# Kernel optimization log

Hardware: AMD Instinct MI355X
Metric: run time of the kernel (lower is better)

Reference implementation:

```python
import jax, jax.numpy as jnp
import numpy as np

M, K, N = 131072, 1024, 512


def setup_inputs() -> dict:
    key = jax.random.key(0)
    k1, k2, k3, k4, k5 = jax.random.split(key, 5)
    scale = 0.02
    return {
        "x": jax.random.normal(k1, (M, K), dtype=jnp.float32),
        "w0": jax.random.uniform(k2, (K,), dtype=jnp.float32, minval=0.9, maxval=1.1),
        "w1": jax.random.normal(k3, (K, N), dtype=jnp.float32) * scale,
        "w2": jax.random.normal(k4, (K, N), dtype=jnp.float32) * scale,
        "w3": jax.random.normal(k5, (N, K), dtype=jnp.float32) * scale,
    }


def reference(x, w0, w1, w2, w3):
    # RMSNorm (no eps, matching the kernel): l = rsqrt(mean(x^2))
    l = jax.lax.rsqrt(jnp.sum(x * x, axis=-1) / K)          # [M]
    x1 = x * l[:, None] * w0[None, :]                        # [M, K]
    x2 = x1 @ w1                                             # gate   [M, N]
    y2 = x1 @ w2                                             # up     [M, N]
    x3 = jax.nn.silu(x2) * y2                                # SiLU-gate [M, N]
    out = x3 @ w3                                            # down   [M, K] (skip_connection=False)
    return out
```

## Files before the change

### kernel.cpp

```cpp
#include <hip/hip_runtime.h>
#include <cstdint>

typedef __attribute__((ext_vector_type(4))) float f32x4;
typedef __attribute__((ext_vector_type(8))) short bf16x8;
typedef __attribute__((ext_vector_type(4))) short bf16x4;

#define DEV static __device__ __forceinline__

DEV unsigned short f2bf(float f) {
    union { float f; unsigned int u; } v; v.f = f;
    unsigned int u = v.u;
    return (unsigned short)((u + 0x7FFFu + ((u >> 16) & 1u)) >> 16);
}

DEV void async_cp16(const void* g, void* l) {
    __builtin_amdgcn_global_load_lds(
        (const __attribute__((address_space(1))) unsigned int*)g,
        (__attribute__((address_space(3))) unsigned int*)l,
        16, 0, 0);
}

#define BAR __builtin_amdgcn_s_barrier();
#define SCB __builtin_amdgcn_sched_barrier(0);
#define LGKM0 asm volatile("s_waitcnt lgkmcnt(0)");
#define P1 __builtin_amdgcn_s_setprio(1);
#define P0 __builtin_amdgcn_s_setprio(0);
#define VM0 asm volatile("s_waitcnt vmcnt(0)" ::: "memory");
#define VM2 asm volatile("s_waitcnt vmcnt(2)" ::: "memory");
#define VM3 asm volatile("s_waitcnt vmcnt(3)" ::: "memory");

DEV void stage_A32(const unsigned short* __restrict__ g, long kofs,
                   unsigned short* l, int tid, int gp) {
#pragma unroll
    for (int i = 0; i < 2; ++i) {
        int c = i * 512 + tid;
        int row = c >> 2;
        int ss = (c & 3) ^ ((row >> 1) & 3);
        async_cp16(g + (long)row * gp + kofs + ss * 8,
                   l + (i * 512 + (tid & 448)) * 8);
    }
}
DEV void stage_B32(const unsigned short* __restrict__ g, long kofs,
                   unsigned short* l, int tid, int gp) {
    int row = tid >> 2;
    int ss = (tid & 3) ^ ((row >> 1) & 3);
    async_cp16(g + (long)row * gp + kofs + ss * 8, l + (tid & 448) * 8);
}

template <int NT>
DEV void gemmB(const unsigned short* __restrict__ gA,
               const unsigned short* __restrict__ gB,
               const int gpa, const int gpb, unsigned short* lds,
               f32x4 (&acc)[4][4], const int tid) {
    const int lane = tid & 63;
    const int wv = tid >> 6;
    const int wr = wv >> 1, wc = wv & 1;
    const int lhi = lane >> 4, llo = lane & 15;
    const int sw = (lhi ^ ((llo >> 1) & 3)) << 3;
    const int aoff = (wr * 64 + llo) * 32 + sw;
    const int boff = (wc * 64 + llo) * 32 + sw;

    unsigned short *pa0 = lds, *pa1 = lds + 8192, *pa2 = lds + 16384;
    unsigned short *pb0 = lds + 24576, *pb1 = lds + 28672;

#define MGJ(J)                                                                \
    _Pragma("unroll") for (int i = 0; i < 4; ++i)                             \
    _Pragma("unroll") for (int jj = 0; jj < 2; ++jj)                          \
        acc[i][(J) + jj] = __builtin_amdgcn_mfma_f32_16x16x32_bf16(           \
            af[i], bf[(J) + jj], acc[i][(J) + jj], 0, 0, 0);

    stage_A32(gA, 0, pa0, tid, gpa);
    stage_B32(gB, 0, pb0, tid, gpb);
    stage_A32(gA, 32, pa1, tid, gpa);
    stage_B32(gB, 32, pb1, tid, gpb);
    VM3
    BAR SCB

    bf16x8 af[4], bf[4];
    for (int t = 0; t < NT; ++t) {
        const bool pf1 = (t + 1 < NT);
        const bool pf2 = (t + 2 < NT);
#pragma unroll
        for (int i = 0; i < 4; ++i) af[i] = *(const bf16x8*)&pa0[aoff + i * 512];
        bf[0] = *(const bf16x8*)&pb0[boff];
        bf[1] = *(const bf16x8*)&pb0[boff + 512];
        if (t >= 1 && pf1) stage_B32(gB, (long)(t + 1) * 32, pb1, tid, gpb);
        BAR LGKM0 SCB
        P1 MGJ(0) P0
        BAR
        bf[2] = *(const bf16x8*)&pb0[boff + 1024];
        bf[3] = *(const bf16x8*)&pb0[boff + 1536];
        if (pf2) stage_A32(gA, (long)(t + 2) * 32, pa2, tid, gpa);
        BAR LGKM0 SCB
        P1 MGJ(2) P0
        if (pf1) { if (pf2) { VM2 } else { VM0 } }
        BAR SCB
        unsigned short* tp = pa0; pa0 = pa1; pa1 = pa2; pa2 = tp;
        tp = pb0; pb0 = pb1; pb1 = tp;
    }
#undef MGJ
}

__global__ void prep_w(const float* __restrict__ w0, const float* __restrict__ w1,
                       const float* __restrict__ w2, const float* __restrict__ w3,
                       unsigned short* __restrict__ w12t, unsigned short* __restrict__ w3t) {
    int t = blockIdx.x * 256 + threadIdx.x;
    if (t < 1048576) {
        int n = t >> 10, k = t & 1023;
        const float* src = (n & 1) ? w2 : w1;
        w12t[t] = f2bf(w0[k] * src[k * 512 + (n >> 1)]);
    } else {
        int idx = t - 1048576;
        int j = idx >> 9, n = idx & 511;
        w3t[idx] = f2bf(w3[n * 1024 + j]);
    }
}

__global__ __launch_bounds__(256)
void prep_x(const float* __restrict__ x, unsigned short* __restrict__ xb) {
    const int wv = threadIdx.x >> 6, lane = threadIdx.x & 63;
    const int stride = gridDim.x * 4;
    for (int row = blockIdx.x * 4 + wv; row < 131072; row += stride) {
        const float* xr = x + (long)row * 1024;
        f32x4 v[4];
        float s = 0.f;
#pragma unroll
        for (int c = 0; c < 4; ++c) {
            v[c] = *(const f32x4*)(xr + c * 256 + lane * 4);
            s += v[c].x * v[c].x + v[c].y * v[c].y + v[c].z * v[c].z + v[c].w * v[c].w;
        }
#pragma unroll
        for (int off = 32; off > 0; off >>= 1) s += __shfl_xor(s, off, 64);
        float l = rsqrtf(s * (1.0f / 1024.0f));
        unsigned short* xo = xb + (long)row * 1024;
#pragma unroll
        for (int c = 0; c < 4; ++c) {
            bf16x4 b;
            b.x = (short)f2bf(v[c].x * l);
            b.y = (short)f2bf(v[c].y * l);
            b.z = (short)f2bf(v[c].z * l);
            b.w = (short)f2bf(v[c].w * l);
            *(bf16x4*)(xo + c * 256 + lane * 4) = b;
        }
    }
}

__global__ __launch_bounds__(512, 4)
void gate_gemm(const unsigned short* __restrict__ xb,
               const unsigned short* __restrict__ w12t,
               unsigned short* __restrict__ x3) {
    __shared__ unsigned short lds[32768];
    const int tid = threadIdx.x;
    const int lane = tid & 63;
    const int wv = tid >> 6;
    const int wr = wv >> 1, wc = wv & 1;
    const int lhi = lane >> 4, llo = lane & 15;

    int bid = blockIdx.x;
    int wgid = (bid & 7) * 512 + (bid >> 3);
    const int mt = wgid >> 3, nt = wgid & 7;

    f32x4 acc[4][4];
#pragma unroll
    for (int i = 0; i < 4; ++i)
#pragma unroll
        for (int j = 0; j < 4; ++j) acc[i][j] = (f32x4){0.f, 0.f, 0.f, 0.f};

    gemmB<32>(xb + (long)mt * 256 * 1024, w12t + (long)nt * 128 * 1024,
              1024, 1024, lds, acc, tid);

#pragma unroll
    for (int i = 0; i < 4; ++i)
#pragma unroll
        for (int rr = 0; rr < 4; ++rr) {
            int R = wr * 64 + i * 16 + lhi * 4 + rr;
#pragma unroll
            for (int j = 0; j < 4; ++j) {
                float v = acc[i][j][rr];
                float p = __shfl_xor(v, 1, 64);
                float g = (lane & 1) ? p : v;
                float u = (lane & 1) ? v : p;
                float s = (g / (1.0f + __expf(-g))) * u;
                if (!(lane & 1))
                    lds[R * 72 + wc * 32 + j * 8 + (llo >> 1)] = f2bf(s);
            }
        }
    __syncthreads();
    unsigned short* xg = x3 + (long)(mt * 256) * 512 + nt * 64;
#pragma unroll
    for (int i = 0; i < 4; ++i) {
        int c = i * 512 + tid;
        int row = c >> 3, ch = c & 7;
        *(bf16x8*)(xg + (long)row * 512 + ch * 8) = *(const bf16x8*)&lds[row * 72 + ch * 8];
    }
}

__global__ __launch_bounds__(512, 4)
void down_gemm(const unsigned short* __restrict__ x3,
               const unsigned short* __restrict__ w3t,
               float* __restrict__ out) {
    __shared__ unsigned short lds[32768];
    const int tid = threadIdx.x;
    const int lane = tid & 63;
    const int wv = tid >> 6;
    const int wr = wv >> 1, wc = wv & 1;
    const int lhi = lane >> 4, llo = lane & 15;

    int bid = blockIdx.x;
    int wgid = (bid & 7) * 512 + (bid >> 3);
    const int mt = wgid >> 3, nt = wgid & 7;

    f32x4 acc[4][4];
#pragma unroll
    for (int i = 0; i < 4; ++i)
#pragma unroll
        for (int j = 0; j < 4; ++j) acc[i][j] = (f32x4){0.f, 0.f, 0.f, 0.f};

    gemmB<16>(x3 + (long)mt * 256 * 512, w3t + (long)nt * 128 * 512,
              512, 512, lds, acc, tid);

    float* op = out + (long)(mt * 256) * 1024 + nt * 128;
#pragma unroll
    for (int i = 0; i < 4; ++i)
#pragma unroll
        for (int rr = 0; rr < 4; ++rr) {
            int R = wr * 64 + i * 16 + lhi * 4 + rr;
#pragma unroll
            for (int j = 0; j < 4; ++j)
                op[(long)R * 1024 + wc * 64 + j * 16 + llo] = acc[i][j][rr];
        }
}

extern "C" void kernel_launch(void* const* d_in, const int* in_sizes, int n_in,
                              void* d_out, int out_size, void* d_ws, size_t ws_size,
                              hipStream_t stream) {
    const float* x  = (const float*)d_in[0];
    const float* w0 = (const float*)d_in[1];
    const float* w1 = (const float*)d_in[2];
    const float* w2 = (const float*)d_in[3];
    const float* w3 = (const float*)d_in[4];
    float* out = (float*)d_out;

    unsigned short* w12t = (unsigned short*)d_ws;
    unsigned short* w3t  = w12t + 1024 * 1024;
    unsigned short* x3   = w3t + 1024 * 512;
    unsigned short* xb   = x3 + (size_t)131072 * 512;

    prep_w<<<dim3(6144), dim3(256), 0, stream>>>(w0, w1, w2, w3, w12t, w3t);
    prep_x<<<dim3(2048), dim3(256), 0, stream>>>(x, xb);
    gate_gemm<<<dim3(4096), dim3(512), 0, stream>>>(xb, w12t, x3);
    down_gemm<<<dim3(4096), dim3(512), 0, stream>>>(x3, w3t, out);
}
```

Before: 697.8 us.

## Shrink GEMM workgroup tiles to 128x128 with 4 waves and fewer barriers

Both GEMM kernels now use 256-thread workgroups computing 128x128 output tiles instead of 512 threads over 256x128, doubling the grid and roughly halving LDS per block. A and B staging share one loader, and the per-iteration barrier count drops from four to two by moving the vmcnt wait ahead of the second barrier. The aim is higher occupancy and less synchronisation overhead. The cost is lower data reuse per tile, so more global/L2 traffic for the weight operand, and an added __syncthreads before the epilogue reuses LDS.

```diff
diff --git a/kernel.cpp b/kernel.cpp
--- a/kernel.cpp
+++ b/kernel.cpp
@@ -27,28 +27,22 @@
 #define P0 __builtin_amdgcn_s_setprio(0);
 #define VM0 asm volatile("s_waitcnt vmcnt(0)" ::: "memory");
 #define VM2 asm volatile("s_waitcnt vmcnt(2)" ::: "memory");
-#define VM3 asm volatile("s_waitcnt vmcnt(3)" ::: "memory");
-
-DEV void stage_A32(const unsigned short* __restrict__ g, long kofs,
+#define VM4 asm volatile("s_waitcnt vmcnt(4)" ::: "memory");
+
+DEV void stage_T32(const unsigned short* __restrict__ g, long kofs,
                    unsigned short* l, int tid, int gp) {
 #pragma unroll
     for (int i = 0; i < 2; ++i) {
-        int c = i * 512 + tid;
+        int c = i * 256 + tid;
         int row = c >> 2;
         int ss = (c & 3) ^ ((row >> 1) & 3);
         async_cp16(g + (long)row * gp + kofs + ss * 8,
-                   l + (i * 512 + (tid & 448)) * 8);
-    }
-}
-DEV void stage_B32(const unsigned short* __restrict__ g, long kofs,
-                   unsigned short* l, int tid, int gp) {
-    int row = tid >> 2;
-    int ss = (tid & 3) ^ ((row >> 1) & 3);
-    async_cp16(g + (long)row * gp + kofs + ss * 8, l + (tid & 448) * 8);
+                   l + (i * 256 + (tid & 192)) * 8);
+    }
 }
 
 template <int NT>
-DEV void gemmB(const unsigned short* __restrict__ gA,
+DEV void gemmC(const unsigned short* __restrict__ gA,
                const unsigned short* __restrict__ gB,
                const int gpa, const int gpb, unsigned short* lds,
                f32x4 (&acc)[4][4], const int tid) {
@@ -60,8 +54,8 @@
     const int aoff = (wr * 64 + llo) * 32 + sw;
     const int boff = (wc * 64 + llo) * 32 + sw;
 
-    unsigned short *pa0 = lds, *pa1 = lds + 8192, *pa2 = lds + 16384;
-    unsigned short *pb0 = lds + 24576, *pb1 = lds + 28672;
+    unsigned short *pa0 = lds, *pa1 = lds + 4096, *pa2 = lds + 8192;
+    unsigned short *pb0 = lds + 12288, *pb1 = lds + 16384;
 
 #define MGJ(J)                                                                \
     _Pragma("unroll") for (int i = 0; i < 4; ++i)                             \
@@ -69,11 +63,11 @@
         acc[i][(J) + jj] = __builtin_amdgcn_mfma_f32_16x16x32_bf16(           \
             af[i], bf[(J) + jj], acc[i][(J) + jj], 0, 0, 0);
 
-    stage_A32(gA, 0, pa0, tid, gpa);
-    stage_B32(gB, 0, pb0, tid, gpb);
-    stage_A32(gA, 32, pa1, tid, gpa);
-    stage_B32(gB, 32, pb1, tid, gpb);
-    VM3
+    stage_T32(gA, 0, pa0, tid, gpa);
+    stage_T32(gB, 0, pb0, tid, gpb);
+    stage_T32(gA, 32, pa1, tid, gpa);
+    stage_T32(gB, 32, pb1, tid, gpb);
+    VM4
     BAR SCB
 
     bf16x8 af[4], bf[4];
@@ -84,17 +78,15 @@
         for (int i = 0; i < 4; ++i) af[i] = *(const bf16x8*)&pa0[aoff + i * 512];
         bf[0] = *(const bf16x8*)&pb0[boff];
         bf[1] = *(const bf16x8*)&pb0[boff + 512];
-        if (t >= 1 && pf1) stage_B32(gB, (long)(t + 1) * 32, pb1, tid, gpb);
+        if (t >= 1 && pf1) stage_T32(gB, (long)(t + 1) * 32, pb1, tid, gpb);
         BAR LGKM0 SCB
         P1 MGJ(0) P0
-        BAR
         bf[2] = *(const bf16x8*)&pb0[boff + 1024];
         bf[3] = *(const bf16x8*)&pb0[boff + 1536];
-        if (pf2) stage_A32(gA, (long)(t + 2) * 32, pa2, tid, gpa);
+        if (pf2) stage_T32(gA, (long)(t + 2) * 32, pa2, tid, gpa);
+        if (pf1) { if (pf2) { VM2 } else { VM0 } }
         BAR LGKM0 SCB
         P1 MGJ(2) P0
-        if (pf1) { if (pf2) { VM2 } else { VM0 } }
-        BAR SCB
         unsigned short* tp = pa0; pa0 = pa1; pa1 = pa2; pa2 = tp;
         tp = pb0; pb0 = pb1; pb1 = tp;
     }
@@ -145,11 +137,11 @@
     }
 }
 
-__global__ __launch_bounds__(512, 4)
+__global__ __launch_bounds__(256, 4)
 void gate_gemm(const unsigned short* __restrict__ xb,
                const unsigned short* __restrict__ w12t,
                unsigned short* __restrict__ x3) {
-    __shared__ unsigned short lds[32768];
+    __shared__ unsigned short lds[20480];
     const int tid = threadIdx.x;
     const int lane = tid & 63;
     const int wv = tid >> 6;
@@ -157,7 +149,7 @@
     const int lhi = lane >> 4, llo = lane & 15;
 
     int bid = blockIdx.x;
-    int wgid = (bid & 7) * 512 + (bid >> 3);
+    int wgid = (bid & 7) * 1024 + (bid >> 3);
     const int mt = wgid >> 3, nt = wgid & 7;
 
     f32x4 acc[4][4];
@@ -166,9 +158,10 @@
 #pragma unroll
         for (int j = 0; j < 4; ++j) acc[i][j] = (f32x4){0.f, 0.f, 0.f, 0.f};
 
-    gemmB<32>(xb + (long)mt * 256 * 1024, w12t + (long)nt * 128 * 1024,
+    gemmC<32>(xb + (long)mt * 128 * 1024, w12t + (long)nt * 128 * 1024,
               1024, 1024, lds, acc, tid);
 
+    __syncthreads();
 #pragma unroll
     for (int i = 0; i < 4; ++i)
 #pragma unroll
@@ -186,20 +179,20 @@
             }
         }
     __syncthreads();
-    unsigned short* xg = x3 + (long)(mt * 256) * 512 + nt * 64;
+    unsigned short* xg = x3 + (long)(mt * 128) * 512 + nt * 64;
 #pragma unroll
     for (int i = 0; i < 4; ++i) {
-        int c = i * 512 + tid;
+        int c = i * 256 + tid;
         int row = c >> 3, ch = c & 7;
         *(bf16x8*)(xg + (long)row * 512 + ch * 8) = *(const bf16x8*)&lds[row * 72 + ch * 8];
     }
 }
 
-__global__ __launch_bounds__(512, 4)
+__global__ __launch_bounds__(256, 4)
 void down_gemm(const unsigned short* __restrict__ x3,
                const unsigned short* __restrict__ w3t,
                float* __restrict__ out) {
-    __shared__ unsigned short lds[32768];
+    __shared__ unsigned short lds[20480];
     const int tid = threadIdx.x;
     const int lane = tid & 63;
     const int wv = tid >> 6;
@@ -207,7 +200,7 @@
     const int lhi = lane >> 4, llo = lane & 15;
 
     int bid = blockIdx.x;
-    int wgid = (bid & 7) * 512 + (bid >> 3);
+    int wgid = (bid & 7) * 1024 + (bid >> 3);
     const int mt = wgid >> 3, nt = wgid & 7;
 
     f32x4 acc[4][4];
@@ -216,10 +209,10 @@
 #pragma unroll
         for (int j = 0; j < 4; ++j) acc[i][j] = (f32x4){0.f, 0.f, 0.f, 0.f};
 
-    gemmB<16>(x3 + (long)mt * 256 * 512, w3t + (long)nt * 128 * 512,
+    gemmC<16>(x3 + (long)mt * 128 * 512, w3t + (long)nt * 128 * 512,
               512, 512, lds, acc, tid);
 
-    float* op = out + (long)(mt * 256) * 1024 + nt * 128;
+    float* op = out + (long)(mt * 128) * 1024 + nt * 128;
 #pragma unroll
     for (int i = 0; i < 4; ++i)
 #pragma unroll
@@ -248,6 +241,6 @@
 
     prep_w<<<dim3(6144), dim3(256), 0, stream>>>(w0, w1, w2, w3, w12t, w3t);
     prep_x<<<dim3(2048), dim3(256), 0, stream>>>(x, xb);
-    gate_gemm<<<dim3(4096), dim3(512), 0, stream>>>(xb, w12t, x3);
-    down_gemm<<<dim3(4096), dim3(512), 0, stream>>>(x3, w3t, out);
-}
+    gate_gemm<<<dim3(8192), dim3(256), 0, stream>>>(xb, w12t, x3);
+    down_gemm<<<dim3(8192), dim3(256), 0, stream>>>(x3, w3t, out);
+}
```

Measured after the change: 727.4 us. +4.2%, slower.
